# Optimization experiments

Hardware: AMD Instinct MI355X
Metric: run time of the kernel (lower is better)

Reference implementation:

```python
import jax, jax.numpy as jnp
import numpy as np

N, H, B = 1048576, 128, 4096


def setup_inputs() -> dict:
    key = jax.random.key(0)
    ks = jax.random.split(key, 10)
    x = jax.random.normal(ks[0], (N, H), dtype=jnp.float32)
    # sorted segment ids with every segment nonempty (matches torch.bincount/split usage)
    batch = jnp.sort(jnp.concatenate([
        jnp.arange(B, dtype=jnp.int32),
        jax.random.randint(ks[1], (N - B,), 0, B, dtype=jnp.int32),
    ]))
    s = 1.0 / np.sqrt(H)
    u = lambda k, shp: jax.random.uniform(k, shp, jnp.float32, -s, s)
    return {
        'session_embedding': x,
        'batch': batch,
        'W1': u(ks[2], (H, H)), 'b1': u(ks[3], (H,)),
        'W2': u(ks[4], (H, H)), 'b2': u(ks[5], (H,)),
        'Wq': u(ks[6], (1, H)), 'bq': u(ks[7], (1,)),
        'W3': u(ks[8], (H, 2 * H)), 'b3': u(ks[9], (H,)),
    }


def reference(session_embedding, batch, W1, b1, W2, b2, Wq, bq, W3, b3):
    # index of the last node in each session (batch is sorted)
    last_idx = jax.ops.segment_max(jnp.arange(N, dtype=jnp.int32), batch, num_segments=B)  # [B]
    v_n = session_embedding[last_idx]                      # [B, H]
    v_n_rep = v_n[batch]                                   # [N, H] last-node broadcast per node
    # attention logits: q(sigmoid(W1 v_n + W2 v_i))
    gate = jax.nn.sigmoid(v_n_rep @ W1.T + b1 + session_embedding @ W2.T + b2)  # [N, H]
    alpha = gate @ Wq.T + bq                               # [N, 1]
    s_g = jax.ops.segment_sum(alpha * session_embedding, batch, num_segments=B)  # [B, H]
    s_h = jnp.concatenate([v_n, s_g], axis=1) @ W3.T + b3  # [B, H]
    return s_h
```

## Files before the change

### kernel.cpp

```cpp
#include <hip/hip_runtime.h>
#include <hip/hip_bf16.h>

#define N_NODES 1048576
#define H 128
#define B_SESS 4096
#define TILE 64

typedef __attribute__((ext_vector_type(8))) short bf16x8;
typedef __attribute__((ext_vector_type(4))) short bf16x4;
typedef __attribute__((ext_vector_type(4))) float f32x4;

__device__ inline short bc(float f) {
  return (short)__builtin_bit_cast(unsigned short, __float2bfloat16(f));
}

__global__ void k_prep(const int* __restrict__ batch, int* __restrict__ last_idx,
                       const float* __restrict__ W2, unsigned short* __restrict__ W2s,
                       float* __restrict__ s_g) {
  int i = blockIdx.x * 256 + threadIdx.x;
  if (i < N_NODES) {
    if (i == N_NODES - 1 || batch[i] != batch[i + 1]) last_idx[batch[i]] = i;
  }
  if (i < B_SESS * H) s_g[i] = 0.f;
  if (i < 2048) {
    int row = i >> 4, u = i & 15;
    const float* src = W2 + row * 128 + u * 8;
    float4 a = *reinterpret_cast<const float4*>(src);
    float4 b = *reinterpret_cast<const float4*>(src + 4);
    bf16x8 o;
    o[0] = bc(a.x); o[1] = bc(a.y); o[2] = bc(a.z); o[3] = bc(a.w);
    o[4] = bc(b.x); o[5] = bc(b.y); o[6] = bc(b.z); o[7] = bc(b.w);
    int up = u ^ (row & 7);
    *reinterpret_cast<bf16x8*>(W2s + row * 128 + up * 8) = o;
  }
}

__global__ void k_apre(const float* __restrict__ x, const int* __restrict__ last_idx,
                       const float* __restrict__ W1, const float* __restrict__ b1,
                       const float* __restrict__ b2, float* __restrict__ A_pre) {
  __shared__ float Wl[128][132];
  __shared__ float vn[8][128];
  int t = threadIdx.x;
  for (int i = 0; i < 16; ++i) {
    int e = (t + i * 256) * 4;
    int r = e >> 7, c = e & 127;
    float4 v = *reinterpret_cast<const float4*>(W1 + e);
    Wl[r][c] = v.x; Wl[r][c + 1] = v.y; Wl[r][c + 2] = v.z; Wl[r][c + 3] = v.w;
  }
  int b0 = blockIdx.x * 8;
  for (int i = t; i < 8 * 128; i += 256) {
    int s = i >> 7, c = i & 127;
    vn[s][c] = x[(size_t)last_idx[b0 + s] * H + c];
  }
  __syncthreads();
  int h = t & 127, si = t >> 7;
  float bias = b1[h] + b2[h];
  for (int s = si; s < 8; s += 2) {
    float acc = bias;
    #pragma unroll
    for (int k = 0; k < 128; k += 4) {
      float4 w = *reinterpret_cast<const float4*>(&Wl[h][k]);
      acc += vn[s][k] * w.x + vn[s][k + 1] * w.y + vn[s][k + 2] * w.z + vn[s][k + 3] * w.w;
    }
    A_pre[(size_t)(b0 + s) * H + h] = acc;
  }
}

__global__ __launch_bounds__(256, 4)
void k_main(const float* __restrict__ x, const int* __restrict__ batch,
            const unsigned short* __restrict__ W2s, const float* __restrict__ Wq,
            const float* __restrict__ bq, const float* __restrict__ A_pre,
            float* __restrict__ s_g) {
  __shared__ unsigned short Wl[128][128];
  __shared__ float apre_s[8][128];
  __shared__ float alph[TILE];
  __shared__ int bsegs[TILE + 1];
  __shared__ float wqs[128];
  int t = threadIdx.x;
  int node0 = blockIdx.x * TILE;
  int w = t >> 6, lane = t & 63, r = lane & 15, ks = lane >> 4;

  #pragma unroll
  for (int i = 0; i < 8; ++i) {
    int seg = w * 8 + i;
    __builtin_amdgcn_global_load_lds(
        reinterpret_cast<const unsigned int*>(
            reinterpret_cast<const char*>(W2s) + seg * 1024 + lane * 16),
        reinterpret_cast<unsigned int*>(
            reinterpret_cast<char*>(&Wl[0][0]) + seg * 1024),
        16, 0, 0);
  }

  float4 af[8];
  const float* xrow = x + (size_t)(node0 + w * 16 + r) * H;
  #pragma unroll
  for (int k = 0; k < 4; ++k) {
    af[2 * k]     = *reinterpret_cast<const float4*>(xrow + k * 32 + ks * 8);
    af[2 * k + 1] = *reinterpret_cast<const float4*>(xrow + k * 32 + ks * 8 + 4);
  }
  int smin = batch[node0];
  int smax = batch[node0 + TILE - 1];
  int cnt = smax - smin + 1;
  bool fast = (cnt <= 8);
  if (fast) {
    const float4* src = reinterpret_cast<const float4*>(A_pre + ((size_t)smin << 7));
    float4* dst = reinterpret_cast<float4*>(&apre_s[0][0]);
    for (int i = t; i < cnt * 32; i += 256) dst[i] = src[i];
  }
  if (t <= TILE) {
    int idx = node0 + t;
    bsegs[t] = (idx < N_NODES) ? batch[idx] : -1;
  }
  if (t < 128) wqs[t] = Wq[t];

  bf16x8 afr[4];
  #pragma unroll
  for (int kg = 0; kg < 4; ++kg) {
    const float* afp = reinterpret_cast<const float*>(af);
    bf16x8 v;
    #pragma unroll
    for (int c = 0; c < 8; ++c) v[c] = bc(afp[kg * 8 + c]);
    afr[kg] = v;
  }
  __syncthreads();

  int sw = r & 7;
  f32x4 acc[8];
  #pragma unroll
  for (int nt = 0; nt < 8; ++nt) acc[nt] = (f32x4){0.f, 0.f, 0.f, 0.f};
  #pragma unroll
  for (int kg = 0; kg < 4; ++kg) {
    int up = (kg * 4 + ks) ^ sw;
    #pragma unroll
    for (int nt = 0; nt < 8; ++nt) {
      bf16x8 b = *reinterpret_cast<const bf16x8*>(&Wl[nt * 16 + r][up * 8]);
      acc[nt] = __builtin_amdgcn_mfma_f32_16x16x32_bf16(afr[kg], b, acc[nt], 0, 0, 0);
    }
  }

  float bqv = bq[0];
  float pa[4];
#define DO_ALPHA(GET) do {                                                   \
    _Pragma("unroll")                                                        \
    for (int j = 0; j < 4; ++j) {                                            \
      int row = bsegs[w * 16 + ks * 4 + j];                                  \
      float s = 0.f;                                                         \
      _Pragma("unroll")                                                      \
      for (int nt = 0; nt < 8; ++nt) {                                       \
        int col = nt * 16 + r;                                               \
        float z = acc[nt][j] + (GET);                                        \
        float g = 1.0f / (1.0f + __expf(-z));                                \
        s += g * wqs[col];                                                   \
      }                                                                      \
      s += __shfl_xor(s, 1); s += __shfl_xor(s, 2);                          \
      s += __shfl_xor(s, 4); s += __shfl_xor(s, 8);                          \
      pa[j] = s + bqv;                                                       \
    } } while (0)
  if (fast) DO_ALPHA(apre_s[row - smin][col]);
  else      DO_ALPHA(A_pre[(size_t)row * H + col]);
#undef DO_ALPHA
  if (r == 0) {
    #pragma unroll
    for (int j = 0; j < 4; ++j) alph[w * 16 + ks * 4 + j] = pa[j];
  }

  int h = t & 127, grp = t >> 7;
  int base = grp * 32;
  const float* xp = x + (size_t)(node0 + base) * H + h;
  float xv[32];
  #pragma unroll
  for (int n = 0; n < 32; ++n) xv[n] = xp[(size_t)n * H];
  __syncthreads();

  float accum = 0.f;
  #pragma unroll
  for (int n = 0; n < 32; ++n) {
    int ln = base + n;
    accum += alph[ln] * xv[n];
    if (bsegs[ln] != bsegs[ln + 1]) {
      atomicAdd(&s_g[((size_t)bsegs[ln] << 7) + h], accum);
      accum = 0.f;
    }
  }
  if (accum != 0.f) atomicAdd(&s_g[((size_t)bsegs[base + 31] << 7) + h], accum);
}

__global__ void k_final(const float* __restrict__ x, const int* __restrict__ last_idx,
                        const float* __restrict__ s_g, const float* __restrict__ W3,
                        const float* __restrict__ b3, float* __restrict__ out) {
  __shared__ float Wl[128][132];
  __shared__ float vin[8][256];
  int t = threadIdx.x;
  int b0 = blockIdx.x * 8;
  for (int i = t; i < 8 * 256; i += 256) {
    int s = i >> 8, c = i & 255;
    float v;
    if (c < 128) v = x[(size_t)last_idx[b0 + s] * H + c];
    else         v = s_g[(size_t)(b0 + s) * H + (c - 128)];
    vin[s][c] = v;
  }
  int h = t & 127, si = t >> 7;
  float res[4];
  for (int half = 0; half < 2; ++half) {
    __syncthreads();
    for (int i = 0; i < 16; ++i) {
      int e = (t + i * 256) * 4;
      int r = e >> 7, c = e & 127;
      float4 v = *reinterpret_cast<const float4*>(W3 + (size_t)r * 256 + half * 128 + c);
      Wl[r][c] = v.x; Wl[r][c + 1] = v.y; Wl[r][c + 2] = v.z; Wl[r][c + 3] = v.w;
    }
    __syncthreads();
    #pragma unroll
    for (int sI = 0; sI < 4; ++sI) {
      int s = si + sI * 2;
      float acc = 0.f;
      #pragma unroll
      for (int k = 0; k < 128; k += 4) {
        float4 wv = *reinterpret_cast<const float4*>(&Wl[h][k]);
        acc += vin[s][half * 128 + k] * wv.x + vin[s][half * 128 + k + 1] * wv.y +
               vin[s][half * 128 + k + 2] * wv.z + vin[s][half * 128 + k + 3] * wv.w;
      }
      if (half == 0) res[sI] = acc;
      else out[(size_t)(b0 + s) * H + h] = res[sI] + acc + b3[h];
    }
  }
}

extern "C" void kernel_launch(void* const* d_in, const int* in_sizes, int n_in,
                              void* d_out, int out_size, void* d_ws, size_t ws_size,
                              hipStream_t stream) {
  const float* x     = (const float*)d_in[0];
  const int*   batch = (const int*)d_in[1];
  const float* W1    = (const float*)d_in[2];
  const float* b1    = (const float*)d_in[3];
  const float* W2    = (const float*)d_in[4];
  const float* b2    = (const float*)d_in[5];
  const float* Wq    = (const float*)d_in[6];
  const float* bq    = (const float*)d_in[7];
  const float* W3    = (const float*)d_in[8];
  const float* b3    = (const float*)d_in[9];
  float* out = (float*)d_out;

  char* ws = (char*)d_ws;
  int*            last_idx = (int*)ws;
  float*          A_pre    = (float*)(ws + 16384);
  float*          s_g      = (float*)(ws + 16384 + 2097152);
  unsigned short* W2s      = (unsigned short*)(ws + 16384 + 2 * 2097152);

  k_prep<<<N_NODES / 256, 256, 0, stream>>>(batch, last_idx, W2, W2s, s_g);
  k_apre<<<B_SESS / 8, 256, 0, stream>>>(x, last_idx, W1, b1, b2, A_pre);
  k_main<<<N_NODES / TILE, 256, 0, stream>>>(x, batch, W2s, Wq, bq, A_pre, s_g);
  k_final<<<B_SESS / 8, 256, 0, stream>>>(x, last_idx, s_g, W3, b3, out);
}
```

Baseline: 220.9 us.

## Process four tiles per block with prefetch of next tile's x and segment data

k_main now loops over four 64-node tiles per block and double-buffers the segment ids, A_pre rows and alpha values. It prefetches the next tile's x fragment into registers while the current tile runs its MFMAs. This spreads the cost of loading W2 into LDS over more work and overlaps global loads with compute. It also drops the XOR swizzle on the W2 LDS layout, which may add bank conflicts, and shrinks the fast-path A_pre cache from 8 segments to 4.

```diff
diff --git a/kernel.cpp b/kernel.cpp
--- a/kernel.cpp
+++ b/kernel.cpp
@@ -5,6 +5,7 @@
 #define H 128
 #define B_SESS 4096
 #define TILE 64
+#define TPB 4
 
 typedef __attribute__((ext_vector_type(8))) short bf16x8;
 typedef __attribute__((ext_vector_type(4))) short bf16x4;
@@ -15,23 +16,18 @@
 }
 
 __global__ void k_prep(const int* __restrict__ batch, int* __restrict__ last_idx,
-                       const float* __restrict__ W2, unsigned short* __restrict__ W2s,
+                       const float* __restrict__ W2, unsigned short* __restrict__ W2b,
                        float* __restrict__ s_g) {
   int i = blockIdx.x * 256 + threadIdx.x;
   if (i < N_NODES) {
     if (i == N_NODES - 1 || batch[i] != batch[i + 1]) last_idx[batch[i]] = i;
   }
   if (i < B_SESS * H) s_g[i] = 0.f;
-  if (i < 2048) {
-    int row = i >> 4, u = i & 15;
-    const float* src = W2 + row * 128 + u * 8;
-    float4 a = *reinterpret_cast<const float4*>(src);
-    float4 b = *reinterpret_cast<const float4*>(src + 4);
-    bf16x8 o;
-    o[0] = bc(a.x); o[1] = bc(a.y); o[2] = bc(a.z); o[3] = bc(a.w);
-    o[4] = bc(b.x); o[5] = bc(b.y); o[6] = bc(b.z); o[7] = bc(b.w);
-    int up = u ^ (row & 7);
-    *reinterpret_cast<bf16x8*>(W2s + row * 128 + up * 8) = o;
+  if (i < 4096) {
+    float4 v = *reinterpret_cast<const float4*>(W2 + (size_t)i * 4);
+    bf16x4 o;
+    o[0] = bc(v.x); o[1] = bc(v.y); o[2] = bc(v.z); o[3] = bc(v.w);
+    *reinterpret_cast<bf16x4*>(W2b + (size_t)i * 4) = o;
   }
 }
 
@@ -68,82 +64,107 @@
 
 __global__ __launch_bounds__(256, 4)
 void k_main(const float* __restrict__ x, const int* __restrict__ batch,
-            const unsigned short* __restrict__ W2s, const float* __restrict__ Wq,
+            const unsigned short* __restrict__ W2b, const float* __restrict__ Wq,
             const float* __restrict__ bq, const float* __restrict__ A_pre,
             float* __restrict__ s_g) {
-  __shared__ unsigned short Wl[128][128];
-  __shared__ float apre_s[8][128];
-  __shared__ float alph[TILE];
-  __shared__ int bsegs[TILE + 1];
+  __shared__ unsigned short Wl[128 * 128];
+  __shared__ float apre2[2][4][128];
+  __shared__ float alph2[2][TILE];
+  __shared__ int bseg2[2][TILE + 1];
   __shared__ float wqs[128];
   int t = threadIdx.x;
-  int node0 = blockIdx.x * TILE;
   int w = t >> 6, lane = t & 63, r = lane & 15, ks = lane >> 4;
+  int base0 = blockIdx.x * (TILE * TPB);
 
   #pragma unroll
   for (int i = 0; i < 8; ++i) {
     int seg = w * 8 + i;
     __builtin_amdgcn_global_load_lds(
         reinterpret_cast<const unsigned int*>(
-            reinterpret_cast<const char*>(W2s) + seg * 1024 + lane * 16),
+            reinterpret_cast<const char*>(W2b) + seg * 1024 + lane * 16),
         reinterpret_cast<unsigned int*>(
-            reinterpret_cast<char*>(&Wl[0][0]) + seg * 1024),
+            reinterpret_cast<char*>(&Wl[0]) + seg * 1024),
         16, 0, 0);
   }
+  if (t < 128) wqs[t] = Wq[t];
+  float bqv = bq[0];
 
   float4 af[8];
-  const float* xrow = x + (size_t)(node0 + w * 16 + r) * H;
-  #pragma unroll
-  for (int k = 0; k < 4; ++k) {
-    af[2 * k]     = *reinterpret_cast<const float4*>(xrow + k * 32 + ks * 8);
-    af[2 * k + 1] = *reinterpret_cast<const float4*>(xrow + k * 32 + ks * 8 + 4);
-  }
-  int smin = batch[node0];
-  int smax = batch[node0 + TILE - 1];
-  int cnt = smax - smin + 1;
-  bool fast = (cnt <= 8);
-  if (fast) {
-    const float4* src = reinterpret_cast<const float4*>(A_pre + ((size_t)smin << 7));
-    float4* dst = reinterpret_cast<float4*>(&apre_s[0][0]);
-    for (int i = t; i < cnt * 32; i += 256) dst[i] = src[i];
-  }
-  if (t <= TILE) {
-    int idx = node0 + t;
-    bsegs[t] = (idx < N_NODES) ? batch[idx] : -1;
-  }
-  if (t < 128) wqs[t] = Wq[t];
-
-  bf16x8 afr[4];
-  #pragma unroll
-  for (int kg = 0; kg < 4; ++kg) {
-    const float* afp = reinterpret_cast<const float*>(af);
-    bf16x8 v;
-    #pragma unroll
-    for (int c = 0; c < 8; ++c) v[c] = bc(afp[kg * 8 + c]);
-    afr[kg] = v;
+  {
+    const float* xrow = x + (size_t)(base0 + w * 16 + r) * H;
+    #pragma unroll
+    for (int k = 0; k < 4; ++k) {
+      af[2 * k]     = *reinterpret_cast<const float4*>(xrow + k * 32 + ks * 8);
+      af[2 * k + 1] = *reinterpret_cast<const float4*>(xrow + k * 32 + ks * 8 + 4);
+    }
+    if (t <= TILE) {
+      int idx = base0 + t;
+      bseg2[0][t] = (idx < N_NODES) ? batch[idx] : -1;
+    }
+    int s0 = batch[base0], s1 = batch[base0 + TILE - 1];
+    int cnt = s1 - s0 + 1;
+    if (cnt <= 4) {
+      const float4* src = reinterpret_cast<const float4*>(A_pre + ((size_t)s0 << 7));
+      float4* dst = reinterpret_cast<float4*>(&apre2[0][0][0]);
+      for (int i = t; i < cnt * 32; i += 256) dst[i] = src[i];
+    }
   }
   __syncthreads();
 
-  int sw = r & 7;
-  f32x4 acc[8];
-  #pragma unroll
-  for (int nt = 0; nt < 8; ++nt) acc[nt] = (f32x4){0.f, 0.f, 0.f, 0.f};
-  #pragma unroll
-  for (int kg = 0; kg < 4; ++kg) {
-    int up = (kg * 4 + ks) ^ sw;
-    #pragma unroll
-    for (int nt = 0; nt < 8; ++nt) {
-      bf16x8 b = *reinterpret_cast<const bf16x8*>(&Wl[nt * 16 + r][up * 8]);
-      acc[nt] = __builtin_amdgcn_mfma_f32_16x16x32_bf16(afr[kg], b, acc[nt], 0, 0, 0);
-    }
-  }
-
-  float bqv = bq[0];
-  float pa[4];
+  for (int tt = 0; tt < TPB; ++tt) {
+    int par = tt & 1;
+    int node0 = base0 + tt * TILE;
+
+    bf16x8 afr[4];
+    #pragma unroll
+    for (int kg = 0; kg < 4; ++kg) {
+      const float* afp = reinterpret_cast<const float*>(af);
+      bf16x8 v;
+      #pragma unroll
+      for (int c = 0; c < 8; ++c) v[c] = bc(afp[kg * 8 + c]);
+      afr[kg] = v;
+    }
+
+    if (tt + 1 < TPB) {
+      const float* xrow = x + (size_t)(node0 + TILE + w * 16 + r) * H;
+      #pragma unroll
+      for (int k = 0; k < 4; ++k) {
+        af[2 * k]     = *reinterpret_cast<const float4*>(xrow + k * 32 + ks * 8);
+        af[2 * k + 1] = *reinterpret_cast<const float4*>(xrow + k * 32 + ks * 8 + 4);
+      }
+      if (t <= TILE) {
+        int idx = node0 + TILE + t;
+        bseg2[par ^ 1][t] = (idx < N_NODES) ? batch[idx] : -1;
+      }
+      int s0 = batch[node0 + TILE], s1 = batch[node0 + TILE + TILE - 1];
+      int cnt = s1 - s0 + 1;
+      if (cnt <= 4) {
+        const float4* src = reinterpret_cast<const float4*>(A_pre + ((size_t)s0 << 7));
+        float4* dst = reinterpret_cast<float4*>(&apre2[par ^ 1][0][0]);
+        for (int i = t; i < cnt * 32; i += 256) dst[i] = src[i];
+      }
+    }
+
+    f32x4 acc[8];
+    #pragma unroll
+    for (int nt = 0; nt < 8; ++nt) acc[nt] = (f32x4){0.f, 0.f, 0.f, 0.f};
+    #pragma unroll
+    for (int kg = 0; kg < 4; ++kg) {
+      #pragma unroll
+      for (int nt = 0; nt < 8; ++nt) {
+        bf16x8 b = *reinterpret_cast<const bf16x8*>(
+            &Wl[(nt * 16 + r) * 128 + kg * 32 + ks * 8]);
+        acc[nt] = __builtin_amdgcn_mfma_f32_16x16x32_bf16(afr[kg], b, acc[nt], 0, 0, 0);
+      }
+    }
+
+    int smin = bseg2[par][0];
+    bool fast = (bseg2[par][TILE - 1] - smin) <= 3;
+    float pa[4];
 #define DO_ALPHA(GET) do {                                                   \
     _Pragma("unroll")                                                        \
     for (int j = 0; j < 4; ++j) {                                            \
-      int row = bsegs[w * 16 + ks * 4 + j];                                  \
+      int row = bseg2[par][w * 16 + ks * 4 + j];                             \
       float s = 0.f;                                                         \
       _Pragma("unroll")                                                      \
       for (int nt = 0; nt < 8; ++nt) {                                       \
@@ -156,33 +177,40 @@
       s += __shfl_xor(s, 4); s += __shfl_xor(s, 8);                          \
       pa[j] = s + bqv;                                                       \
     } } while (0)
-  if (fast) DO_ALPHA(apre_s[row - smin][col]);
-  else      DO_ALPHA(A_pre[(size_t)row * H + col]);
+    if (fast) DO_ALPHA(apre2[par][row - smin][col]);
+    else      DO_ALPHA(A_pre[(size_t)row * H + col]);
 #undef DO_ALPHA
-  if (r == 0) {
-    #pragma unroll
-    for (int j = 0; j < 4; ++j) alph[w * 16 + ks * 4 + j] = pa[j];
-  }
-
-  int h = t & 127, grp = t >> 7;
-  int base = grp * 32;
-  const float* xp = x + (size_t)(node0 + base) * H + h;
-  float xv[32];
-  #pragma unroll
-  for (int n = 0; n < 32; ++n) xv[n] = xp[(size_t)n * H];
-  __syncthreads();
-
-  float accum = 0.f;
-  #pragma unroll
-  for (int n = 0; n < 32; ++n) {
-    int ln = base + n;
-    accum += alph[ln] * xv[n];
-    if (bsegs[ln] != bsegs[ln + 1]) {
-      atomicAdd(&s_g[((size_t)bsegs[ln] << 7) + h], accum);
-      accum = 0.f;
-    }
-  }
-  if (accum != 0.f) atomicAdd(&s_g[((size_t)bsegs[base + 31] << 7) + h], accum);
+    if (r == 0) {
+      #pragma unroll
+      for (int j = 0; j < 4; ++j) alph2[par][w * 16 + ks * 4 + j] = pa[j];
+    }
+    __syncthreads();
+
+    {
+      int h = t & 127, grp = t >> 7;
+      int base = grp * 32;
+      const float* xp = x + (size_t)(node0 + base) * H + h;
+      float accum = 0.f;
+      #pragma unroll
+      for (int c = 0; c < 2; ++c) {
+        float xvv[16];
+        #pragma unroll
+        for (int n = 0; n < 16; ++n) xvv[n] = xp[(size_t)(c * 16 + n) * H];
+        #pragma unroll
+        for (int n = 0; n < 16; ++n) {
+          int ln = base + c * 16 + n;
+          accum += alph2[par][ln] * xvv[n];
+          if (bseg2[par][ln] != bseg2[par][ln + 1]) {
+            atomicAdd(&s_g[((size_t)bseg2[par][ln] << 7) + h], accum);
+            accum = 0.f;
+          }
+        }
+      }
+      if (accum != 0.f)
+        atomicAdd(&s_g[((size_t)bseg2[par][base + 31] << 7) + h], accum);
+    }
+    __syncthreads();
+  }
 }
 
 __global__ void k_final(const float* __restrict__ x, const int* __restrict__ last_idx,
@@ -245,10 +273,10 @@
   int*            last_idx = (int*)ws;
   float*          A_pre    = (float*)(ws + 16384);
   float*          s_g      = (float*)(ws + 16384 + 2097152);
-  unsigned short* W2s      = (unsigned short*)(ws + 16384 + 2 * 2097152);
-
-  k_prep<<<N_NODES / 256, 256, 0, stream>>>(batch, last_idx, W2, W2s, s_g);
+  unsigned short* W2b      = (unsigned short*)(ws + 16384 + 2 * 2097152);
+
+  k_prep<<<N_NODES / 256, 256, 0, stream>>>(batch, last_idx, W2, W2b, s_g);
   k_apre<<<B_SESS / 8, 256, 0, stream>>>(x, last_idx, W1, b1, b2, A_pre);
-  k_main<<<N_NODES / TILE, 256, 0, stream>>>(x, batch, W2s, Wq, bq, A_pre, s_g);
+  k_main<<<N_NODES / (TILE * TPB), 256, 0, stream>>>(x, batch, W2b, Wq, bq, A_pre, s_g);
   k_final<<<B_SESS / 8, 256, 0, stream>>>(x, last_idx, s_g, W3, b3, out);
 }
```

After: 255.0 us. 15.4% more time.
